# Kernel tuning notes

Hardware: AMD Instinct MI355X
Metric: run time of the kernel (lower is better)

## Reference

```python
import jax, jax.numpy as jnp
import numpy as np

D = 8           # spatial size of conv feature map
K = 24          # conv channels
Q = 128         # question embedding size
IN_SIZE = 2 * (K + 2) + Q  # 180
HID = 256
OUT = 28


def _coords(d):
    # faithful to torch float-tensor arithmetic: a/d is float division
    a = jnp.arange(d * d, dtype=jnp.float32)
    cx = (a / d - d / 2) / (d / 2.0)
    cy = (a % d - d / 2) / (d / 2.0)
    return jnp.stack([cx, cy], axis=1)  # [d^2, 2]


def setup_inputs() -> dict:
    key = jax.random.key(0)
    ks = jax.random.split(key, 16)
    s = 0.05
    inp = {
        "x": jax.random.normal(ks[0], (64, K, D, D), dtype=jnp.float32),
        "qst": jax.random.normal(ks[1], (64, Q), dtype=jnp.float32),
        # g MLP (weights stored [in, out])
        "g1_w": jax.random.normal(ks[2], (IN_SIZE, HID), dtype=jnp.float32) * s,
        "g1_b": jnp.zeros((HID,), dtype=jnp.float32),
        "g2_w": jax.random.normal(ks[3], (HID, HID), dtype=jnp.float32) * s,
        "g2_b": jnp.zeros((HID,), dtype=jnp.float32),
        "g3_w": jax.random.normal(ks[4], (HID, HID), dtype=jnp.float32) * s,
        "g3_b": jnp.zeros((HID,), dtype=jnp.float32),
        "g4_w": jax.random.normal(ks[5], (HID, HID), dtype=jnp.float32) * s,
        "g4_b": jnp.zeros((HID,), dtype=jnp.float32),
        # f MLP
        "f1_w": jax.random.normal(ks[6], (HID, HID), dtype=jnp.float32) * s,
        "f1_b": jnp.zeros((HID,), dtype=jnp.float32),
        "f2_w": jax.random.normal(ks[7], (HID, HID), dtype=jnp.float32) * s,
        "f2_b": jnp.zeros((HID,), dtype=jnp.float32),
        "f3_w": jax.random.normal(ks[8], (HID, OUT), dtype=jnp.float32) * s,
        "f3_b": jnp.zeros((OUT,), dtype=jnp.float32),
    }
    return inp


def _forward(x, qst, g1_w, g1_b, g2_w, g2_b, g3_w, g3_b, g4_w, g4_b,
             f1_w, f1_b, f2_w, f2_b, f3_w, f3_b):
    b, k, d, _ = x.shape
    n = d * d  # 64 objects
    # [b, n, k] object features + 2 coord channels -> [b, n, 26]
    xf = jnp.transpose(x.reshape(b, k, n), (0, 2, 1))
    ct = jnp.broadcast_to(_coords(d)[None], (b, n, 2))
    xf = jnp.concatenate([xf, ct], axis=2)                      # [b, n, 26]
    obj = k + 2
    # x_i: varies along axis 2 (original torch layout); x_j varies along axis 1 and carries qst
    xi = jnp.broadcast_to(xf[:, None, :, :], (b, n, n, obj))
    xjq = jnp.concatenate(
        [xf, jnp.broadcast_to(qst[:, None, :], (b, n, qst.shape[1]))], axis=2)
    xj = jnp.broadcast_to(xjq[:, :, None, :], (b, n, n, obj + qst.shape[1]))
    pair = jnp.concatenate([xi, xj], axis=3)                    # [b, n, n, 180]
    # g MLP over all pairs
    h = jax.nn.relu(pair @ g1_w + g1_b)
    h = jax.nn.relu(h @ g2_w + g2_b)
    h = jax.nn.relu(h @ g3_w + g3_b)
    h = jax.nn.relu(h @ g4_w + g4_b)                            # [b, n, n, 256]
    xg = jnp.sum(h, axis=(1, 2))                                # sum over d^4 pairs
    # f MLP (dropout is identity in eval mode)
    xf_ = jax.nn.relu(xg @ f1_w + f1_b)
    xf_ = jax.nn.relu(xf_ @ f2_w + f2_b)
    logits = xf_ @ f3_w + f3_b
    return jax.nn.log_softmax(logits, axis=-1)


def reference(x, qst, g1_w, g1_b, g2_w, g2_b, g3_w, g3_b, g4_w, g4_b,
              f1_w, f1_b, f2_w, f2_b, f3_w, f3_b):
    return _forward(x, qst, g1_w, g1_b, g2_w, g2_b, g3_w, g3_b, g4_w, g4_b,
                    f1_w, f1_b, f2_w, f2_b, f3_w, f3_b)
```

## Files before the change

kernel.cpp:

```cpp
#include <hip/hip_runtime.h>

typedef __bf16 bf16_t;
typedef __bf16 bf16x8 __attribute__((ext_vector_type(8)));
typedef __bf16 bf16x4 __attribute__((ext_vector_type(4)));
typedef float  f32x4  __attribute__((ext_vector_type(4)));


__device__ __forceinline__ int swz(int row, int col) {
  return (((col >> 3) ^ (row & 7)) << 3) | (col & 7);
}

__global__ __launch_bounds__(256) void rn_prep_kernel(
    const float* __restrict__ x, const float* __restrict__ qst,
    const float* __restrict__ g1w, const float* __restrict__ g1b,
    const float* __restrict__ g2w, const float* __restrict__ g3w,
    const float* __restrict__ g4w,
    float* __restrict__ A, float* __restrict__ C,
    bf16_t* __restrict__ Wt, float* __restrict__ xg)
{
  __shared__ float T[64][65];
  int blk = blockIdx.x;
  int n   = threadIdx.x;
  if (blk < 256) {
    int b  = blk >> 2;
    int jg = (blk & 3) * 16;
    float accQ = g1b[n];
    const float* qb = qst + b * 128;
    #pragma unroll 8
    for (int qi = 0; qi < 128; ++qi)
      accQ += qb[qi] * g1w[(52 + qi) * 256 + n];

    float w24 = g1w[24 * 256 + n], w25 = g1w[25 * 256 + n];
    float w50 = g1w[50 * 256 + n], w51 = g1w[51 * 256 + n];
    float accA[16], accC[16];
    #pragma unroll
    for (int t = 0; t < 16; ++t) {
      int j = jg + t;
      float cx = ((float)j * 0.125f - 4.0f) * 0.25f;
      float cy = ((float)(j & 7) - 4.0f) * 0.25f;
      accA[t] = cx * w24 + cy * w25;
      accC[t] = accQ + cx * w50 + cy * w51;
    }
    for (int c = 0; c < 24; ++c) {
      float wa = g1w[c * 256 + n];
      float wc = g1w[(26 + c) * 256 + n];
      const float* xc = x + (b * 24 + c) * 64 + jg;
      #pragma unroll
      for (int t = 0; t < 16; ++t) {
        float xv = xc[t];
        accA[t] += xv * wa;
        accC[t] += xv * wc;
      }
    }
    #pragma unroll
    for (int t = 0; t < 16; ++t) {
      A[(b * 64 + jg + t) * 256 + n] = accA[t];
      C[(b * 64 + jg + t) * 256 + n] = accC[t];
    }
  } else if (blk < 256 + 48) {
    int t   = blk - 256;
    int mat = t >> 4;
    int tl  = t & 15;
    int kt  = (tl & 3) * 64;
    int nt_ = (tl >> 2) * 64;
    const float* W = (mat == 0) ? g2w : (mat == 1 ? g3w : g4w);
    int lane = n & 63, w = n >> 6;
    #pragma unroll
    for (int it = 0; it < 16; ++it) {
      int kl = w * 16 + it;
      T[kl][lane] = W[(kt + kl) * 256 + nt_ + lane];
    }
    __syncthreads();
    #pragma unroll
    for (int it = 0; it < 16; ++it) {
      int nl = w * 16 + it;
      Wt[mat * 65536 + (nt_ + nl) * 256 + kt + lane] = (bf16_t)T[lane][nl];
    }
  } else {
    int idx = (blk - (256 + 48)) * 256 + n;
    xg[idx] = 0.f;
  }
}

__global__ __launch_bounds__(256, 2) void rn_main_kernel(
    const float* __restrict__ A, const float* __restrict__ C,
    const bf16_t* __restrict__ Wt,
    const float* __restrict__ g2b, const float* __restrict__ g3b,
    const float* __restrict__ g4b,
    float* __restrict__ xg)
{
  __shared__ bf16_t hbuf[128][256];

  int tid  = threadIdx.x;
  int bx   = blockIdx.x;
  int b    = bx >> 5;
  int ip   = bx & 31;
  int lane = tid & 63;
  int wave = tid >> 6;
  int n0   = wave * 64;

  {
    const float* Ab = A + (size_t)b * 64 * 256;
    const float* Cr = C + ((size_t)b * 64 + ip * 2) * 256;
    #pragma unroll
    for (int it = 0; it < 16; ++it) {
      int g = it * 256 + tid;
      int j = g >> 6;
      int n = (g & 63) * 4;
      const float4 a4 = *(const float4*)(Ab + j * 256 + n);
      const float4 c0 = *(const float4*)(Cr + n);
      const float4 c1 = *(const float4*)(Cr + 256 + n);
      bf16x4 v0, v1;
      v0[0] = (bf16_t)fmaxf(a4.x + c0.x, 0.f);
      v0[1] = (bf16_t)fmaxf(a4.y + c0.y, 0.f);
      v0[2] = (bf16_t)fmaxf(a4.z + c0.z, 0.f);
      v0[3] = (bf16_t)fmaxf(a4.w + c0.w, 0.f);
      v1[0] = (bf16_t)fmaxf(a4.x + c1.x, 0.f);
      v1[1] = (bf16_t)fmaxf(a4.y + c1.y, 0.f);
      v1[2] = (bf16_t)fmaxf(a4.z + c1.z, 0.f);
      v1[3] = (bf16_t)fmaxf(a4.w + c1.w, 0.f);
      *(bf16x4*)&hbuf[j][swz(j, n)] = v0;
      *(bf16x4*)&hbuf[64 + j][swz(64 + j, n)] = v1;
    }
  }

  const float* biases[3] = {g2b, g3b, g4b};
  int r = lane & 15;
  int q = lane >> 4;

  for (int L = 0; L < 3; ++L) {
    __syncthreads();
    const bf16_t* W = Wt + L * 65536;
    const float* bias = biases[L];

    f32x4 acc[4][8];
    #pragma unroll
    for (int nt = 0; nt < 4; ++nt)
      #pragma unroll
      for (int mt = 0; mt < 8; ++mt)
        #pragma unroll
        for (int e = 0; e < 4; ++e) acc[nt][mt][e] = 0.f;

    #pragma unroll
    for (int ks = 0; ks < 8; ++ks) {
      int k0 = ks * 32 + q * 8;
      bf16x8 wf[4], hf[8];
      #pragma unroll
      for (int nt = 0; nt < 4; ++nt)
        wf[nt] = *(const bf16x8*)&W[(n0 + nt * 16 + r) * 256 + k0];
      #pragma unroll
      for (int mt = 0; mt < 8; ++mt) {
        int row = mt * 16 + r;
        hf[mt] = *(const bf16x8*)&hbuf[row][swz(row, k0)];
      }
      #pragma unroll
      for (int nt = 0; nt < 4; ++nt)
        #pragma unroll
        for (int mt = 0; mt < 8; ++mt)
          acc[nt][mt] = __builtin_amdgcn_mfma_f32_16x16x32_bf16(
              wf[nt], hf[mt], acc[nt][mt], 0, 0, 0);
    }

    float4 bv[4];
    #pragma unroll
    for (int nt = 0; nt < 4; ++nt)
      bv[nt] = *(const float4*)&bias[n0 + nt * 16 + q * 4];

    if (L < 2) {
      __syncthreads();
      #pragma unroll
      for (int nt = 0; nt < 4; ++nt) {
        int col = n0 + nt * 16 + q * 4;
        #pragma unroll
        for (int mt = 0; mt < 8; ++mt) {
          int row = mt * 16 + r;
          bf16x4 v;
          v[0] = (bf16_t)fmaxf(acc[nt][mt][0] + bv[nt].x, 0.f);
          v[1] = (bf16_t)fmaxf(acc[nt][mt][1] + bv[nt].y, 0.f);
          v[2] = (bf16_t)fmaxf(acc[nt][mt][2] + bv[nt].z, 0.f);
          v[3] = (bf16_t)fmaxf(acc[nt][mt][3] + bv[nt].w, 0.f);
          *(bf16x4*)&hbuf[row][swz(row, col)] = v;
        }
      }
    } else {
      #pragma unroll
      for (int nt = 0; nt < 4; ++nt) {
        float p0 = 0.f, p1 = 0.f, p2 = 0.f, p3 = 0.f;
        #pragma unroll
        for (int mt = 0; mt < 8; ++mt) {
          p0 += fmaxf(acc[nt][mt][0] + bv[nt].x, 0.f);
          p1 += fmaxf(acc[nt][mt][1] + bv[nt].y, 0.f);
          p2 += fmaxf(acc[nt][mt][2] + bv[nt].z, 0.f);
          p3 += fmaxf(acc[nt][mt][3] + bv[nt].w, 0.f);
        }
        #pragma unroll
        for (int d = 1; d < 16; d <<= 1) {
          p0 += __shfl_xor(p0, d, 64);
          p1 += __shfl_xor(p1, d, 64);
          p2 += __shfl_xor(p2, d, 64);
          p3 += __shfl_xor(p3, d, 64);
        }
        if (r == 0) {
          int n = b * 256 + n0 + nt * 16 + q * 4;
          atomicAdd(&xg[n + 0], p0);
          atomicAdd(&xg[n + 1], p1);
          atomicAdd(&xg[n + 2], p2);
          atomicAdd(&xg[n + 3], p3);
        }
      }
    }
  }
}

__global__ __launch_bounds__(256) void rn_f_kernel(
    const float* __restrict__ xg,
    const float* __restrict__ f1w, const float* __restrict__ f1b,
    const float* __restrict__ f2w, const float* __restrict__ f2b,
    const float* __restrict__ f3w, const float* __restrict__ f3b,
    float* __restrict__ out)
{
  __shared__ float xs[256], t1[256], t2[256], lg[28], lse[1];
  int b = blockIdx.x, tid = threadIdx.x;
  xs[tid] = xg[b * 256 + tid];
  __syncthreads();
  float acc = f1b[tid];
  for (int k = 0; k < 256; ++k) acc += xs[k] * f1w[k * 256 + tid];
  t1[tid] = fmaxf(acc, 0.f);
  __syncthreads();
  acc = f2b[tid];
  for (int k = 0; k < 256; ++k) acc += t1[k] * f2w[k * 256 + tid];
  t2[tid] = fmaxf(acc, 0.f);
  __syncthreads();
  if (tid < 28) {
    float a2 = f3b[tid];
    for (int k = 0; k < 256; ++k) a2 += t2[k] * f3w[k * 28 + tid];
    lg[tid] = a2;
  }
  __syncthreads();
  if (tid == 0) {
    float m = lg[0];
    for (int j = 1; j < 28; ++j) m = fmaxf(m, lg[j]);
    float se = 0.f;
    for (int j = 0; j < 28; ++j) se += expf(lg[j] - m);
    lse[0] = m + logf(se);
  }
  __syncthreads();
  if (tid < 28) out[b * 28 + tid] = lg[tid] - lse[0];
}

extern "C" void kernel_launch(void* const* d_in, const int* in_sizes, int n_in,
                              void* d_out, int out_size, void* d_ws, size_t ws_size,
                              hipStream_t stream) {
  (void)in_sizes; (void)n_in; (void)out_size; (void)ws_size;
  const float* x   = (const float*)d_in[0];
  const float* qst = (const float*)d_in[1];
  const float* g1w = (const float*)d_in[2];
  const float* g1b = (const float*)d_in[3];
  const float* g2w = (const float*)d_in[4];
  const float* g2b = (const float*)d_in[5];
  const float* g3w = (const float*)d_in[6];
  const float* g3b = (const float*)d_in[7];
  const float* g4w = (const float*)d_in[8];
  const float* g4b = (const float*)d_in[9];
  const float* f1w = (const float*)d_in[10];
  const float* f1b = (const float*)d_in[11];
  const float* f2w = (const float*)d_in[12];
  const float* f2b = (const float*)d_in[13];
  const float* f3w = (const float*)d_in[14];
  const float* f3b = (const float*)d_in[15];
  float* out = (float*)d_out;

  float*  A  = (float*)d_ws;
  float*  C  = A + 4096 * 256;
  bf16_t* Wt = (bf16_t*)(C + 4096 * 256);
  float*  xg = (float*)((char*)Wt + 3 * 65536 * sizeof(bf16_t));

  rn_prep_kernel<<<256 + 48 + 64, 256, 0, stream>>>(
      x, qst, g1w, g1b, g2w, g3w, g4w, A, C, Wt, xg);
  rn_main_kernel<<<2048, 256, 0, stream>>>(A, C, Wt, g2b, g3b, g4b, xg);
  rn_f_kernel<<<64, 256, 0, stream>>>(xg, f1w, f1b, f2w, f2b, f3w, f3b, out);
}
```

Measured before the change: 253.4 us.

## Halve per-block pair tile to 64 rows, double grid, and remap block order

Each main-kernel block now handles one i row (64 pairs) instead of two, halving LDS and accumulator registers so occupancy hint rises to 4 blocks per SIMD-set and the grid doubles to 4096. Block indices are remapped so consecutive blocks spread across batches, which changes cache locality and atomic contention patterns. The trade-off is that weight fragments are reloaded from global/L2 twice as often per pair, and the number of atomics into xg doubles.

```diff
diff --git a/kernel.cpp b/kernel.cpp
--- a/kernel.cpp
+++ b/kernel.cpp
@@ -82,81 +82,75 @@
   }
 }
 
-__global__ __launch_bounds__(256, 2) void rn_main_kernel(
+__global__ __launch_bounds__(256, 4) void rn_main_kernel(
     const float* __restrict__ A, const float* __restrict__ C,
     const bf16_t* __restrict__ Wt,
     const float* __restrict__ g2b, const float* __restrict__ g3b,
     const float* __restrict__ g4b,
     float* __restrict__ xg)
 {
-  __shared__ bf16_t hbuf[128][256];
+  __shared__ bf16_t hbuf[64][256];
 
   int tid  = threadIdx.x;
-  int bx   = blockIdx.x;
-  int b    = bx >> 5;
-  int ip   = bx & 31;
+  int bx0  = blockIdx.x;
+  int bx   = (bx0 & 7) * 512 + (bx0 >> 3);
+  int b    = bx >> 6;
+  int i    = bx & 63;
   int lane = tid & 63;
   int wave = tid >> 6;
   int n0   = wave * 64;
+  int r    = lane & 15;
+  int q    = lane >> 4;
 
   {
     const float* Ab = A + (size_t)b * 64 * 256;
-    const float* Cr = C + ((size_t)b * 64 + ip * 2) * 256;
+    const float* Cr = C + ((size_t)b * 64 + i) * 256;
+    int n = lane * 4;
+    const float4 c4 = *(const float4*)(Cr + n);
     #pragma unroll
     for (int it = 0; it < 16; ++it) {
-      int g = it * 256 + tid;
-      int j = g >> 6;
-      int n = (g & 63) * 4;
+      int j = it * 4 + wave;
       const float4 a4 = *(const float4*)(Ab + j * 256 + n);
-      const float4 c0 = *(const float4*)(Cr + n);
-      const float4 c1 = *(const float4*)(Cr + 256 + n);
-      bf16x4 v0, v1;
-      v0[0] = (bf16_t)fmaxf(a4.x + c0.x, 0.f);
-      v0[1] = (bf16_t)fmaxf(a4.y + c0.y, 0.f);
-      v0[2] = (bf16_t)fmaxf(a4.z + c0.z, 0.f);
-      v0[3] = (bf16_t)fmaxf(a4.w + c0.w, 0.f);
-      v1[0] = (bf16_t)fmaxf(a4.x + c1.x, 0.f);
-      v1[1] = (bf16_t)fmaxf(a4.y + c1.y, 0.f);
-      v1[2] = (bf16_t)fmaxf(a4.z + c1.z, 0.f);
-      v1[3] = (bf16_t)fmaxf(a4.w + c1.w, 0.f);
-      *(bf16x4*)&hbuf[j][swz(j, n)] = v0;
-      *(bf16x4*)&hbuf[64 + j][swz(64 + j, n)] = v1;
+      bf16x4 v;
+      v[0] = (bf16_t)fmaxf(a4.x + c4.x, 0.f);
+      v[1] = (bf16_t)fmaxf(a4.y + c4.y, 0.f);
+      v[2] = (bf16_t)fmaxf(a4.z + c4.z, 0.f);
+      v[3] = (bf16_t)fmaxf(a4.w + c4.w, 0.f);
+      *(bf16x4*)&hbuf[j][swz(j, n)] = v;
     }
   }
 
   const float* biases[3] = {g2b, g3b, g4b};
-  int r = lane & 15;
-  int q = lane >> 4;
 
   for (int L = 0; L < 3; ++L) {
     __syncthreads();
     const bf16_t* W = Wt + L * 65536;
     const float* bias = biases[L];
 
-    f32x4 acc[4][8];
+    f32x4 acc[4][4];
     #pragma unroll
     for (int nt = 0; nt < 4; ++nt)
       #pragma unroll
-      for (int mt = 0; mt < 8; ++mt)
+      for (int mt = 0; mt < 4; ++mt)
         #pragma unroll
         for (int e = 0; e < 4; ++e) acc[nt][mt][e] = 0.f;
 
     #pragma unroll
     for (int ks = 0; ks < 8; ++ks) {
       int k0 = ks * 32 + q * 8;
-      bf16x8 wf[4], hf[8];
+      bf16x8 wf[4], hf[4];
       #pragma unroll
       for (int nt = 0; nt < 4; ++nt)
         wf[nt] = *(const bf16x8*)&W[(n0 + nt * 16 + r) * 256 + k0];
       #pragma unroll
-      for (int mt = 0; mt < 8; ++mt) {
+      for (int mt = 0; mt < 4; ++mt) {
         int row = mt * 16 + r;
         hf[mt] = *(const bf16x8*)&hbuf[row][swz(row, k0)];
       }
       #pragma unroll
       for (int nt = 0; nt < 4; ++nt)
         #pragma unroll
-        for (int mt = 0; mt < 8; ++mt)
+        for (int mt = 0; mt < 4; ++mt)
           acc[nt][mt] = __builtin_amdgcn_mfma_f32_16x16x32_bf16(
               wf[nt], hf[mt], acc[nt][mt], 0, 0, 0);
     }
@@ -172,7 +166,7 @@
       for (int nt = 0; nt < 4; ++nt) {
         int col = n0 + nt * 16 + q * 4;
         #pragma unroll
-        for (int mt = 0; mt < 8; ++mt) {
+        for (int mt = 0; mt < 4; ++mt) {
           int row = mt * 16 + r;
           bf16x4 v;
           v[0] = (bf16_t)fmaxf(acc[nt][mt][0] + bv[nt].x, 0.f);
@@ -187,7 +181,7 @@
       for (int nt = 0; nt < 4; ++nt) {
         float p0 = 0.f, p1 = 0.f, p2 = 0.f, p3 = 0.f;
         #pragma unroll
-        for (int mt = 0; mt < 8; ++mt) {
+        for (int mt = 0; mt < 4; ++mt) {
           p0 += fmaxf(acc[nt][mt][0] + bv[nt].x, 0.f);
           p1 += fmaxf(acc[nt][mt][1] + bv[nt].y, 0.f);
           p2 += fmaxf(acc[nt][mt][2] + bv[nt].z, 0.f);
@@ -277,6 +271,6 @@
 
   rn_prep_kernel<<<256 + 48 + 64, 256, 0, stream>>>(
       x, qst, g1w, g1b, g2w, g3w, g4w, A, C, Wt, xg);
-  rn_main_kernel<<<2048, 256, 0, stream>>>(A, C, Wt, g2b, g3b, g4b, xg);
+  rn_main_kernel<<<4096, 256, 0, stream>>>(A, C, Wt, g2b, g3b, g4b, xg);
   rn_f_kernel<<<64, 256, 0, stream>>>(xg, f1w, f1b, f2w, f2b, f3w, f3b, out);
 }
```

Measured after the change: 357.0 us. 40.9% more time.

## Preload fragment-ordered weights into registers and split pair rows into two halves

Applied to the files above, without the earlier changes.

The prep kernel now writes the bf16 g2-g4 weights in MFMA fragment order, so each wave can load its whole 64-column weight slice into registers once per layer with coalesced loads. The old per-k-step global weight fetches go away. The main kernel splits the 128-row activation buffer into two 64-row halves and processes them one after another. This halves the accumulator count to offset the register cost of the held weights, and lets one half's epilogue sit next to the other half's MFMAs. Block indices are remapped to change how work is spread over the device, and C rows are loaded once per thread. The cost is very high register pressure from 32 bf16x8 weight fragments per lane, which risks spills or reduced occupancy.

```diff
diff --git a/kernel.cpp b/kernel.cpp
--- a/kernel.cpp
+++ b/kernel.cpp
@@ -73,8 +73,13 @@
     __syncthreads();
     #pragma unroll
     for (int it = 0; it < 16; ++it) {
-      int nl = w * 16 + it;
-      Wt[mat * 65536 + (nt_ + nl) * 256 + kt + lane] = (bf16_t)T[lane][nl];
+      int nl  = w * 16 + it;
+      int no  = nt_ + nl;
+      int k   = kt + lane;
+      int wv  = no >> 6, rr = no & 15, ntI = (no >> 4) & 3;
+      int ksI = k >> 5,  qI = (k >> 3) & 3, e = k & 7;
+      int idx = ((((wv * 4 + ntI) * 8 + ksI) * 64) + qI * 16 + rr) * 8 + e;
+      Wt[mat * 65536 + idx] = (bf16_t)T[lane][nl];
     }
   } else {
     int idx = (blk - (256 + 48)) * 256 + n;
@@ -89,27 +94,30 @@
     const float* __restrict__ g4b,
     float* __restrict__ xg)
 {
-  __shared__ bf16_t hbuf[128][256];
+  __shared__ bf16_t h0[64][256];
+  __shared__ bf16_t h1[64][256];
 
   int tid  = threadIdx.x;
-  int bx   = blockIdx.x;
+  int bx0  = blockIdx.x;
+  int bx   = (bx0 & 7) * 256 + (bx0 >> 3);
   int b    = bx >> 5;
   int ip   = bx & 31;
   int lane = tid & 63;
   int wave = tid >> 6;
   int n0   = wave * 64;
+  int r    = lane & 15;
+  int q    = lane >> 4;
 
   {
     const float* Ab = A + (size_t)b * 64 * 256;
     const float* Cr = C + ((size_t)b * 64 + ip * 2) * 256;
+    int nn = lane * 4;
+    const float4 c0 = *(const float4*)(Cr + nn);
+    const float4 c1 = *(const float4*)(Cr + 256 + nn);
     #pragma unroll
     for (int it = 0; it < 16; ++it) {
-      int g = it * 256 + tid;
-      int j = g >> 6;
-      int n = (g & 63) * 4;
-      const float4 a4 = *(const float4*)(Ab + j * 256 + n);
-      const float4 c0 = *(const float4*)(Cr + n);
-      const float4 c1 = *(const float4*)(Cr + 256 + n);
+      int j = it * 4 + wave;
+      const float4 a4 = *(const float4*)(Ab + j * 256 + nn);
       bf16x4 v0, v1;
       v0[0] = (bf16_t)fmaxf(a4.x + c0.x, 0.f);
       v0[1] = (bf16_t)fmaxf(a4.y + c0.y, 0.f);
@@ -119,97 +127,131 @@
       v1[1] = (bf16_t)fmaxf(a4.y + c1.y, 0.f);
       v1[2] = (bf16_t)fmaxf(a4.z + c1.z, 0.f);
       v1[3] = (bf16_t)fmaxf(a4.w + c1.w, 0.f);
-      *(bf16x4*)&hbuf[j][swz(j, n)] = v0;
-      *(bf16x4*)&hbuf[64 + j][swz(64 + j, n)] = v1;
-    }
-  }
-
-  const float* biases[3] = {g2b, g3b, g4b};
-  int r = lane & 15;
-  int q = lane >> 4;
-
+      *(bf16x4*)&h0[j][swz(j, nn)] = v0;
+      *(bf16x4*)&h1[j][swz(j, nn)] = v1;
+    }
+  }
+
+#define KS_LOOP(HB, ACC)                                                \
+  {                                                                     \
+    _Pragma("unroll")                                                   \
+    for (int ks = 0; ks < 8; ++ks) {                                    \
+      int k0 = ks * 32 + q * 8;                                         \
+      bf16x8 hf[4];                                                     \
+      _Pragma("unroll")                                                 \
+      for (int mt = 0; mt < 4; ++mt) {                                  \
+        int row = mt * 16 + r;                                          \
+        hf[mt] = *(const bf16x8*)&HB[row][swz(row, k0)];                \
+      }                                                                 \
+      _Pragma("unroll")                                                 \
+      for (int nt = 0; nt < 4; ++nt)                                    \
+        _Pragma("unroll")                                               \
+        for (int mt = 0; mt < 4; ++mt)                                  \
+          ACC[nt][mt] = __builtin_amdgcn_mfma_f32_16x16x32_bf16(        \
+              wreg[nt][ks], hf[mt], ACC[nt][mt], 0, 0, 0);              \
+    }                                                                   \
+  }
+
+#define EPILOGUE(HB, ACC)                                               \
+  {                                                                     \
+    _Pragma("unroll")                                                   \
+    for (int nt = 0; nt < 4; ++nt) {                                    \
+      float4 bv = *(const float4*)&bias[n0 + nt * 16 + q * 4];          \
+      int col = n0 + nt * 16 + q * 4;                                   \
+      _Pragma("unroll")                                                 \
+      for (int mt = 0; mt < 4; ++mt) {                                  \
+        int row = mt * 16 + r;                                          \
+        bf16x4 v;                                                       \
+        v[0] = (bf16_t)fmaxf(ACC[nt][mt][0] + bv.x, 0.f);               \
+        v[1] = (bf16_t)fmaxf(ACC[nt][mt][1] + bv.y, 0.f);               \
+        v[2] = (bf16_t)fmaxf(ACC[nt][mt][2] + bv.z, 0.f);               \
+        v[3] = (bf16_t)fmaxf(ACC[nt][mt][3] + bv.w, 0.f);               \
+        *(bf16x4*)&HB[row][swz(row, col)] = v;                          \
+      }                                                                 \
+    }                                                                   \
+  }
+
+#define REDUCE_ATOMIC(ACC)                                              \
+  {                                                                     \
+    _Pragma("unroll")                                                   \
+    for (int nt = 0; nt < 4; ++nt) {                                    \
+      float4 bv = *(const float4*)&bias[n0 + nt * 16 + q * 4];          \
+      float p0 = 0.f, p1 = 0.f, p2 = 0.f, p3 = 0.f;                     \
+      _Pragma("unroll")                                                 \
+      for (int mt = 0; mt < 4; ++mt) {                                  \
+        p0 += fmaxf(ACC[nt][mt][0] + bv.x, 0.f);                        \
+        p1 += fmaxf(ACC[nt][mt][1] + bv.y, 0.f);                        \
+        p2 += fmaxf(ACC[nt][mt][2] + bv.z, 0.f);                        \
+        p3 += fmaxf(ACC[nt][mt][3] + bv.w, 0.f);                        \
+      }                                                                 \
+      _Pragma("unroll")                                                 \
+      for (int d = 1; d < 16; d <<= 1) {                                \
+        p0 += __shfl_xor(p0, d, 64);                                    \
+        p1 += __shfl_xor(p1, d, 64);                                    \
+        p2 += __shfl_xor(p2, d, 64);                                    \
+        p3 += __shfl_xor(p3, d, 64);                                    \
+      }                                                                 \
+      if (r == 0) {                                                     \
+        int nn = b * 256 + n0 + nt * 16 + q * 4;                        \
+        atomicAdd(&xg[nn + 0], p0);                                     \
+        atomicAdd(&xg[nn + 1], p1);                                     \
+        atomicAdd(&xg[nn + 2], p2);                                     \
+        atomicAdd(&xg[nn + 3], p3);                                     \
+      }                                                                 \
+    }                                                                   \
+  }
+
+  #pragma unroll
   for (int L = 0; L < 3; ++L) {
-    __syncthreads();
-    const bf16_t* W = Wt + L * 65536;
-    const float* bias = biases[L];
-
-    f32x4 acc[4][8];
+    const bf16_t* Wl = Wt + L * 65536 + wave * 16384;
+    bf16x8 wreg[4][8];
     #pragma unroll
     for (int nt = 0; nt < 4; ++nt)
       #pragma unroll
-      for (int mt = 0; mt < 8; ++mt)
-        #pragma unroll
-        for (int e = 0; e < 4; ++e) acc[nt][mt][e] = 0.f;
-
-    #pragma unroll
-    for (int ks = 0; ks < 8; ++ks) {
-      int k0 = ks * 32 + q * 8;
-      bf16x8 wf[4], hf[8];
-      #pragma unroll
-      for (int nt = 0; nt < 4; ++nt)
-        wf[nt] = *(const bf16x8*)&W[(n0 + nt * 16 + r) * 256 + k0];
-      #pragma unroll
-      for (int mt = 0; mt < 8; ++mt) {
-        int row = mt * 16 + r;
-        hf[mt] = *(const bf16x8*)&hbuf[row][swz(row, k0)];
-      }
+      for (int ks = 0; ks < 8; ++ks)
+        wreg[nt][ks] = *(const bf16x8*)&Wl[((nt * 8 + ks) * 64 + lane) * 8];
+
+    const float* bias = (L == 0) ? g2b : (L == 1) ? g3b : g4b;
+
+    if (L == 0) __syncthreads();
+
+    {
+      f32x4 acc[4][4];
       #pragma unroll
       for (int nt = 0; nt < 4; ++nt)
         #pragma unroll
-        for (int mt = 0; mt < 8; ++mt)
-          acc[nt][mt] = __builtin_amdgcn_mfma_f32_16x16x32_bf16(
-              wf[nt], hf[mt], acc[nt][mt], 0, 0, 0);
-    }
-
-    float4 bv[4];
-    #pragma unroll
-    for (int nt = 0; nt < 4; ++nt)
-      bv[nt] = *(const float4*)&bias[n0 + nt * 16 + q * 4];
-
-    if (L < 2) {
+        for (int mt = 0; mt < 4; ++mt)
+          #pragma unroll
+          for (int e = 0; e < 4; ++e) acc[nt][mt][e] = 0.f;
+      KS_LOOP(h0, acc)
       __syncthreads();
+      if (L < 2) {
+        EPILOGUE(h0, acc)
+      } else {
+        REDUCE_ATOMIC(acc)
+      }
+    }
+
+    {
+      f32x4 acc[4][4];
       #pragma unroll
-      for (int nt = 0; nt < 4; ++nt) {
-        int col = n0 + nt * 16 + q * 4;
+      for (int nt = 0; nt < 4; ++nt)
         #pragma unroll
-        for (int mt = 0; mt < 8; ++mt) {
-          int row = mt * 16 + r;
-          bf16x4 v;
-          v[0] = (bf16_t)fmaxf(acc[nt][mt][0] + bv[nt].x, 0.f);
-          v[1] = (bf16_t)fmaxf(acc[nt][mt][1] + bv[nt].y, 0.f);
-          v[2] = (bf16_t)fmaxf(acc[nt][mt][2] + bv[nt].z, 0.f);
-          v[3] = (bf16_t)fmaxf(acc[nt][mt][3] + bv[nt].w, 0.f);
-          *(bf16x4*)&hbuf[row][swz(row, col)] = v;
-        }
+        for (int mt = 0; mt < 4; ++mt)
+          #pragma unroll
+          for (int e = 0; e < 4; ++e) acc[nt][mt][e] = 0.f;
+      KS_LOOP(h1, acc)
+      if (L < 2) {
+        __syncthreads();
+        EPILOGUE(h1, acc)
+      } else {
+        REDUCE_ATOMIC(acc)
       }
-    } else {
-      #pragma unroll
-      for (int nt = 0; nt < 4; ++nt) {
-        float p0 = 0.f, p1 = 0.f, p2 = 0.f, p3 = 0.f;
-        #pragma unroll
-        for (int mt = 0; mt < 8; ++mt) {
-          p0 += fmaxf(acc[nt][mt][0] + bv[nt].x, 0.f);
-          p1 += fmaxf(acc[nt][mt][1] + bv[nt].y, 0.f);
-          p2 += fmaxf(acc[nt][mt][2] + bv[nt].z, 0.f);
-          p3 += fmaxf(acc[nt][mt][3] + bv[nt].w, 0.f);
-        }
-        #pragma unroll
-        for (int d = 1; d < 16; d <<= 1) {
-          p0 += __shfl_xor(p0, d, 64);
-          p1 += __shfl_xor(p1, d, 64);
-          p2 += __shfl_xor(p2, d, 64);
-          p3 += __shfl_xor(p3, d, 64);
-        }
-        if (r == 0) {
-          int n = b * 256 + n0 + nt * 16 + q * 4;
-          atomicAdd(&xg[n + 0], p0);
-          atomicAdd(&xg[n + 1], p1);
-          atomicAdd(&xg[n + 2], p2);
-          atomicAdd(&xg[n + 3], p3);
-        }
-      }
-    }
-  }
+    }
+  }
+#undef KS_LOOP
+#undef EPILOGUE
+#undef REDUCE_ATOMIC
 }
 
 __global__ __launch_bounds__(256) void rn_f_kernel(
```

Result: slower. 344.7 us (+36.0%).
